# Kernel tuning notes

Measured on AMD Instinct MI355X. Metric: run time of the kernel, lower is better.

Reference implementation:

```python
import jax, jax.numpy as jnp
import numpy as np

NUM_HEADS = 8
LN_EPS = 1e-5


def layer_norm(x, g, b):
    mu = jnp.mean(x, axis=-1, keepdims=True)
    var = jnp.var(x, axis=-1, keepdims=True)
    return (x - mu) * jax.lax.rsqrt(var + LN_EPS) * g + b


def mha(q, k, v, in_w, in_b, out_w, out_b):
    # torch nn.MultiheadAttention (batch_first): packed in_proj (3D,D), out_proj (D,D)
    B, Lq, D = q.shape
    Lk = k.shape[1]
    H = NUM_HEADS
    dh = D // H
    wq, wk, wv = in_w[:D], in_w[D:2 * D], in_w[2 * D:]
    bq, bk, bv = in_b[:D], in_b[D:2 * D], in_b[2 * D:]
    qp = (q @ wq.T + bq).reshape(B, Lq, H, dh).transpose(0, 2, 1, 3)
    kp = (k @ wk.T + bk).reshape(B, Lk, H, dh).transpose(0, 2, 1, 3)
    vp = (v @ wv.T + bv).reshape(B, Lk, H, dh).transpose(0, 2, 1, 3)
    scores = jnp.einsum('bhqd,bhkd->bhqk', qp, kp) / jnp.sqrt(jnp.asarray(dh, q.dtype))
    attn = jax.nn.softmax(scores, axis=-1)  # (B,H,Lq,Lk)
    out = jnp.einsum('bhqk,bhkd->bhqd', attn, vp)
    out = out.transpose(0, 2, 1, 3).reshape(B, Lq, D)
    return out @ out_w.T + out_b, attn


def setup_inputs() -> dict:
    key = jax.random.key(0)
    ks = jax.random.split(key, 8)
    B, P, Q, D = 32, 576, 256, 768
    s = 0.02
    return {
        'image_tokens': jax.random.normal(ks[0], (B, 1 + P, D), jnp.float32),
        'tactile_tokens': jax.random.normal(ks[1], (B, Q, D), jnp.float32),
        't2i_in_w': jax.random.normal(ks[2], (3 * D, D), jnp.float32) * s,
        't2i_in_b': jnp.zeros((3 * D,), jnp.float32),
        't2i_out_w': jax.random.normal(ks[3], (D, D), jnp.float32) * s,
        't2i_out_b': jnp.zeros((D,), jnp.float32),
        'i2t_in_w': jax.random.normal(ks[4], (3 * D, D), jnp.float32) * s,
        'i2t_in_b': jnp.zeros((3 * D,), jnp.float32),
        'i2t_out_w': jax.random.normal(ks[5], (D, D), jnp.float32) * s,
        'i2t_out_b': jnp.zeros((D,), jnp.float32),
        'ln_tact_g': jnp.ones((D,), jnp.float32),
        'ln_tact_b': jnp.zeros((D,), jnp.float32),
        'ln_img_g': jnp.ones((D,), jnp.float32),
        'ln_img_b': jnp.zeros((D,), jnp.float32),
    }


def reference(image_tokens, tactile_tokens, t2i_in_w, t2i_in_b, t2i_out_w, t2i_out_b,
              i2t_in_w, i2t_in_b, i2t_out_w, i2t_out_b,
              ln_tact_g, ln_tact_b, ln_img_g, ln_img_b):
    # attention_type == 'all_patch'
    cls_tok = image_tokens[:, :1, :]
    patch_tok = image_tokens[:, 1:, :]
    tact_out, attn_weights = mha(tactile_tokens, patch_tok, patch_tok,
                                 t2i_in_w, t2i_in_b, t2i_out_w, t2i_out_b)
    tactile_tokens = layer_norm(tactile_tokens + tact_out, ln_tact_g, ln_tact_b)
    patch_out, _ = mha(patch_tok, tactile_tokens, tactile_tokens,
                       i2t_in_w, i2t_in_b, i2t_out_w, i2t_out_b)
    patch_tok = layer_norm(patch_tok + patch_out, ln_img_g, ln_img_b)
    image_tokens = jnp.concatenate([cls_tok, patch_tok], axis=1)
    return image_tokens, tactile_tokens, attn_weights
```

## Files before the change

### kernel.cpp

```cpp
#include <hip/hip_runtime.h>
#include <stdint.h>
#include <math.h>

typedef unsigned short u16;
typedef __attribute__((ext_vector_type(8))) short bf16x8;
typedef __attribute__((ext_vector_type(4))) float f32x4;

__device__ __forceinline__ u16 f2b(float f) {
    unsigned u = __float_as_uint(f);
    u = (u + 0x7FFFu + ((u >> 16) & 1u)) >> 16;
    return (u16)u;
}

__device__ __forceinline__ void gload16(const void* g, void* lds) {
    __builtin_amdgcn_global_load_lds(
        (const __attribute__((address_space(1))) unsigned int*)(uintptr_t)g,
        (__attribute__((address_space(3))) unsigned int*)(unsigned int)(uintptr_t)lds,
        16, 0, 0);
}

#define BM 128
#define BN 128
#define BK 32

struct GemmGrp {
    const u16* A; const u16* B; const float* bias; const float* resid;
    float* Cf; u16* Cb;
    int M, N, lda, ldb, ldc;
    float scale;
    int rgrp; long long rgA, rgoff; int ldr;
};
struct G3 { GemmGrp g[3]; int start[4]; int K; };

__global__ __launch_bounds__(256) void gemm_grp(G3 P)
{
    __shared__ __align__(16) u16 lA[2][BM * BK];
    __shared__ __align__(16) u16 lB[2][BN * BK];

    const int tid = threadIdx.x;
    const int wave = tid >> 6;
    const int lane = tid & 63;

    const int ntot = P.start[3];
    int L = blockIdx.x;
    if ((ntot & 7) == 0) L = (L & 7) * (ntot >> 3) + (L >> 3);

    const int gi = (L >= P.start[1]) + (L >= P.start[2]);
    GemmGrp g;
    if (gi == 0) g = P.g[0]; else if (gi == 1) g = P.g[1]; else g = P.g[2];
    const int t = L - P.start[gi];

    const int tilesN = g.N / BN;
    const int tm = t / tilesN;
    const int tn = t % tilesN;
    const int row0 = tm * BM;
    const int col0 = tn * BN;

    const int f0 = tid * 8;
    const int f1 = (256 + tid) * 8;
    const int sr0 = f0 >> 5, sc0 = f0 & 31;
    const int sr1 = f1 >> 5, sc1 = f1 & 31;

    const u16* pa0 = g.A + (long long)(row0 + sr0) * g.lda + sc0;
    const u16* pa1 = g.A + (long long)(row0 + sr1) * g.lda + sc1;
    const u16* pb0 = g.B + (long long)(col0 + sr0) * g.ldb + sc0;
    const u16* pb1 = g.B + (long long)(col0 + sr1) * g.ldb + sc1;

    const int wr = wave >> 1, wc = wave & 1;
    const int fr = lane & 15;
    const int kk = (lane >> 4) * 8;

    f32x4 acc[4][4];
    #pragma unroll
    for (int m = 0; m < 4; ++m)
        #pragma unroll
        for (int n = 0; n < 4; ++n) {
            f32x4 z = {0.f, 0.f, 0.f, 0.f};
            acc[m][n] = z;
        }

    #define STAGE(buf, k0) do { \
        gload16(pa0 + (k0), &lA[buf][(wave * 64) * 8]); \
        gload16(pa1 + (k0), &lA[buf][2048 + (wave * 64) * 8]); \
        gload16(pb0 + (k0), &lB[buf][(wave * 64) * 8]); \
        gload16(pb1 + (k0), &lB[buf][2048 + (wave * 64) * 8]); \
    } while (0)

    STAGE(0, 0);
    __syncthreads();
    int cur = 0;
    for (int k0 = 0; k0 < P.K; k0 += BK) {
        if (k0 + BK < P.K) STAGE(cur ^ 1, k0 + BK);
        bf16x8 af[4], bfv[4];
        #pragma unroll
        for (int m = 0; m < 4; ++m)
            af[m] = *(const bf16x8*)&lA[cur][(wr * 64 + m * 16 + fr) * BK + kk];
        #pragma unroll
        for (int n = 0; n < 4; ++n)
            bfv[n] = *(const bf16x8*)&lB[cur][(wc * 64 + n * 16 + fr) * BK + kk];
        #pragma unroll
        for (int m = 0; m < 4; ++m)
            #pragma unroll
            for (int n = 0; n < 4; ++n)
                acc[m][n] = __builtin_amdgcn_mfma_f32_16x16x32_bf16(af[m], bfv[n], acc[m][n], 0, 0, 0);
        __syncthreads();
        cur ^= 1;
    }
    #undef STAGE

    const int orow = row0 + wr * 64;
    const int ocol = col0 + wc * 64;
    const int g4 = (lane >> 4) * 4;
    float bcol[4];
    #pragma unroll
    for (int n = 0; n < 4; ++n)
        bcol[n] = g.bias ? g.bias[ocol + n * 16 + fr] : 0.f;

    #pragma unroll
    for (int m = 0; m < 4; ++m) {
        #pragma unroll
        for (int j = 0; j < 4; ++j) {
            const int r = orow + m * 16 + g4 + j;
            long long ro = 0;
            if (g.resid) {
                unsigned q = (unsigned)r / (unsigned)g.rgrp;
                unsigned rem = (unsigned)r - q * (unsigned)g.rgrp;
                ro = (long long)q * g.rgA + (long long)rem * g.ldr + g.rgoff;
            }
            const long long crow = (long long)r * g.ldc;
            #pragma unroll
            for (int n = 0; n < 4; ++n) {
                const int c = ocol + n * 16 + fr;
                float v = acc[m][n][j] * g.scale + bcol[n];
                if (g.resid) v += g.resid[ro + c];
                if (g.Cb) g.Cb[crow + c] = f2b(v);
                else      g.Cf[crow + c] = v;
            }
        }
    }
}

template <bool WATTN>
__global__ __launch_bounds__(256, 2) void fused_attn(
    const u16* __restrict__ Q, const u16* __restrict__ K, const u16* __restrict__ Vt,
    float* __restrict__ attn, u16* __restrict__ O,
    int Lq, int Lk, int ldq, int ldk, int ldo)
{
    __shared__ __align__(16) u16 lQP[128 * 96];
    __shared__ __align__(16) u16 lKt[2][64 * 96];
    __shared__ __align__(16) u16 lVt[2][96 * 64];
    __shared__ float lM2[2][128], lL2[2][128];

    const int tid = threadIdx.x, wave = tid >> 6, lane = tid & 63;
    const int fr = lane & 15, g = lane >> 4;
    const int wr = wave >> 1, wc = wave & 1;
    const int z = blockIdx.y, b = z >> 3, h = z & 7;
    const int q0 = blockIdx.x * 128;
    const int nt = Lk >> 6;

    const u16* Qz = Q + (long long)b * Lq * ldq + h * 96;
    const u16* Kz = K + (long long)b * Lk * ldk + h * 96;
    const u16* Vz = Vt + (long long)z * 96 * Lk;
    u16* Oz = O + (long long)b * Lq * ldo + h * 96;
    float* Az = attn + (long long)z * Lq * Lk;

    const u16* qsrc[6];
    #pragma unroll
    for (int t = 0; t < 6; ++t) {
        int u = t * 256 + tid;
        int r = u / 12, cu = u % 12;
        int qr = q0 + r; if (qr > Lq - 1) qr = Lq - 1;
        qsrc[t] = Qz + (long long)qr * ldq + cu * 8;
    }
    const u16* ksrc[3];
    #pragma unroll
    for (int t = 0; t < 3; ++t) {
        int u = t * 256 + tid;
        int r = u / 12, cu = u % 12;
        ksrc[t] = Kz + (long long)r * ldk + cu * 8;
    }
    const u16* vsrc[3];
    #pragma unroll
    for (int t = 0; t < 3; ++t) {
        int u = t * 256 + tid;
        int d = u >> 3, uu = u & 7;
        vsrc[t] = Vz + (long long)d * Lk + ((uu ^ (d & 7)) * 8);
    }
    const long long kstep = 64LL * ldk;

    #define DQ(t)    ((char*)lQP + ((t) * 256 + wave * 64) * 16)
    #define DK(bf,t) ((char*)lKt[bf] + ((t) * 256 + wave * 64) * 16)
    #define DV(bf,t) ((char*)lVt[bf] + ((t) * 256 + wave * 64) * 16)

    #pragma unroll
    for (int t = 0; t < 6; ++t) gload16(qsrc[t], DQ(t));
    #pragma unroll
    for (int t = 0; t < 3; ++t) gload16(ksrc[t], DK(0, t));
    __syncthreads();

    bf16x8 qf[4][3];
    #pragma unroll
    for (int m = 0; m < 4; ++m)
        #pragma unroll
        for (int ks = 0; ks < 3; ++ks)
            qf[m][ks] = *(const bf16x8*)((const char*)lQP + (wr * 64 + m * 16 + fr) * 192 + ks * 64 + g * 16);

    float m_run[4], l_run[4];
    #pragma unroll
    for (int i = 0; i < 4; ++i) { m_run[i] = -1e30f; l_run[i] = 0.f; }

    int buf = 0;
    for (int i = 0; i < nt; ++i) {
        if (i + 1 < nt) {
            #pragma unroll
            for (int t = 0; t < 3; ++t) { ksrc[t] += kstep; gload16(ksrc[t], DK(buf ^ 1, t)); }
        }
        bf16x8 kf[2][3];
        #pragma unroll
        for (int mk = 0; mk < 2; ++mk)
            #pragma unroll
            for (int ks = 0; ks < 3; ++ks)
                kf[mk][ks] = *(const bf16x8*)((const char*)lKt[buf] + (wc * 32 + mk * 16 + fr) * 192 + ks * 64 + g * 16);
        f32x4 sa[2][4];
        #pragma unroll
        for (int mk = 0; mk < 2; ++mk)
            #pragma unroll
            for (int nq = 0; nq < 4; ++nq) {
                f32x4 zz = {0.f, 0.f, 0.f, 0.f};
                sa[mk][nq] = zz;
            }
        __builtin_amdgcn_s_setprio(1);
        #pragma unroll
        for (int ks = 0; ks < 3; ++ks)
            #pragma unroll
            for (int mk = 0; mk < 2; ++mk)
                #pragma unroll
                for (int nq = 0; nq < 4; ++nq)
                    sa[mk][nq] = __builtin_amdgcn_mfma_f32_16x16x32_bf16(kf[mk][ks], qf[nq][ks], sa[mk][nq], 0, 0, 0);
        __builtin_amdgcn_s_setprio(0);
        #pragma unroll
        for (int nq = 0; nq < 4; ++nq) {
            float tmx = -1e30f;
            #pragma unroll
            for (int mk = 0; mk < 2; ++mk)
                #pragma unroll
                for (int j = 0; j < 4; ++j)
                    tmx = fmaxf(tmx, sa[mk][nq][j]);
            tmx = fmaxf(tmx, __shfl_xor(tmx, 16));
            tmx = fmaxf(tmx, __shfl_xor(tmx, 32));
            const float mnew = fmaxf(m_run[nq], tmx);
            float ts = 0.f;
            #pragma unroll
            for (int mk = 0; mk < 2; ++mk)
                #pragma unroll
                for (int j = 0; j < 4; ++j)
                    ts += __expf(sa[mk][nq][j] - mnew);
            ts += __shfl_xor(ts, 16);
            ts += __shfl_xor(ts, 32);
            l_run[nq] = l_run[nq] * __expf(m_run[nq] - mnew) + ts;
            m_run[nq] = mnew;
        }
        __syncthreads();
        buf ^= 1;
    }

    if (g == 0) {
        #pragma unroll
        for (int nq = 0; nq < 4; ++nq) {
            lM2[wc][wr * 64 + nq * 16 + fr] = m_run[nq];
            lL2[wc][wr * 64 + nq * 16 + fr] = l_run[nq];
        }
    }
    #pragma unroll
    for (int t = 0; t < 3; ++t) ksrc[t] -= (long long)(nt - 1) * kstep;
    #pragma unroll
    for (int t = 0; t < 3; ++t) gload16(ksrc[t], DK(0, t));
    #pragma unroll
    for (int t = 0; t < 3; ++t) gload16(vsrc[t], DV(0, t));
    __syncthreads();

    float mrow[16], linv[16];
    #pragma unroll
    for (int m = 0; m < 4; ++m)
        #pragma unroll
        for (int j = 0; j < 4; ++j) {
            const int q = wr * 64 + m * 16 + g * 4 + j;
            const float ma = lM2[0][q], mb = lM2[1][q];
            const float mm = fmaxf(ma, mb);
            const float ll = lL2[0][q] * __expf(ma - mm) + lL2[1][q] * __expf(mb - mm);
            mrow[m * 4 + j] = mm;
            linv[m * 4 + j] = 1.f / ll;
        }

    f32x4 oacc[4][3];
    #pragma unroll
    for (int m = 0; m < 4; ++m)
        #pragma unroll
        for (int nd = 0; nd < 3; ++nd) {
            f32x4 zz = {0.f, 0.f, 0.f, 0.f};
            oacc[m][nd] = zz;
        }

    buf = 0;
    for (int i = 0; i < nt; ++i) {
        const int k0 = i * 64;
        if (i + 1 < nt) {
            #pragma unroll
            for (int t = 0; t < 3; ++t) { ksrc[t] += kstep; gload16(ksrc[t], DK(buf ^ 1, t)); }
            #pragma unroll
            for (int t = 0; t < 3; ++t) { vsrc[t] += 64;    gload16(vsrc[t], DV(buf ^ 1, t)); }
        }
        bf16x8 kf[2][3];
        #pragma unroll
        for (int n = 0; n < 2; ++n)
            #pragma unroll
            for (int ks = 0; ks < 3; ++ks)
                kf[n][ks] = *(const bf16x8*)((const char*)lKt[buf] + (wc * 32 + n * 16 + fr) * 192 + ks * 64 + g * 16);
        f32x4 ss[4][2];
        #pragma unroll
        for (int m = 0; m < 4; ++m)
            #pragma unroll
            for (int n = 0; n < 2; ++n) {
                f32x4 zz = {0.f, 0.f, 0.f, 0.f};
                ss[m][n] = zz;
            }
        __builtin_amdgcn_s_setprio(1);
        #pragma unroll
        for (int ks = 0; ks < 3; ++ks)
            #pragma unroll
            for (int m = 0; m < 4; ++m)
                #pragma unroll
                for (int n = 0; n < 2; ++n)
                    ss[m][n] = __builtin_amdgcn_mfma_f32_16x16x32_bf16(qf[m][ks], kf[n][ks], ss[m][n], 0, 0, 0);
        __builtin_amdgcn_s_setprio(0);
        #pragma unroll
        for (int m = 0; m < 4; ++m)
            #pragma unroll
            for (int n = 0; n < 2; ++n)
                #pragma unroll
                for (int j = 0; j < 4; ++j) {
                    const float p = __expf(ss[m][n][j] - mrow[m * 4 + j]) * linv[m * 4 + j];
                    const int q = wr * 64 + m * 16 + g * 4 + j;
                    const int k = wc * 32 + n * 16 + fr;
                    if (WATTN) Az[(long long)(q0 + q) * Lk + k0 + k] = p;
                    *(u16*)((char*)lQP + q * 144 + k * 2) = f2b(p);
                }
        __syncthreads();
        __builtin_amdgcn_s_setprio(1);
        #pragma unroll
        for (int ks = 0; ks < 2; ++ks) {
            bf16x8 vf[3], pf[4];
            #pragma unroll
            for (int nd = 0; nd < 3; ++nd) {
                const int row = wc * 48 + nd * 16 + fr;
                vf[nd] = *(const bf16x8*)((const char*)lVt[buf] + row * 128 + (((ks * 4 + g) ^ (row & 7)) * 16));
            }
            #pragma unroll
            for (int m = 0; m < 4; ++m)
                pf[m] = *(const bf16x8*)((const char*)lQP + (wr * 64 + m * 16 + fr) * 144 + ks * 64 + g * 16);
            #pragma unroll
            for (int m = 0; m < 4; ++m)
                #pragma unroll
                for (int nd = 0; nd < 3; ++nd)
                    oacc[m][nd] = __builtin_amdgcn_mfma_f32_16x16x32_bf16(pf[m], vf[nd], oacc[m][nd], 0, 0, 0);
        }
        __builtin_amdgcn_s_setprio(0);
        __syncthreads();
        buf ^= 1;
    }

    #pragma unroll
    for (int m = 0; m < 4; ++m)
        #pragma unroll
        for (int j = 0; j < 4; ++j) {
            const int q = q0 + wr * 64 + m * 16 + g * 4 + j;
            if (q < Lq) {
                #pragma unroll
                for (int nd = 0; nd < 3; ++nd) {
                    const int c = wc * 48 + nd * 16 + fr;
                    Oz[(long long)q * ldo + c] = f2b(oacc[m][nd][j]);
                }
            }
        }
    #undef DQ
    #undef DK
    #undef DV
}

__global__ __launch_bounds__(256) void transpose_v(
    const u16* __restrict__ V, u16* __restrict__ Vt, int L, int ldv)
{
    __shared__ unsigned int t[64 * 97];
    const int z = blockIdx.y;
    const int b = z >> 3, h = z & 7;
    const int l0 = blockIdx.x * 64;
    const int tid = threadIdx.x;
    for (int i = 0; i < 24; ++i) {
        const int idx = tid + i * 256;
        const int l = idx / 96, d = idx % 96;
        t[l * 97 + d] = V[((long long)(b * L + l0 + l)) * ldv + h * 96 + d];
    }
    __syncthreads();
    for (int i = 0; i < 24; ++i) {
        const int idx = tid + i * 256;
        const int d = idx / 64, l = idx % 64;
        Vt[((long long)z * 96 + d) * L + l0 + l] = (u16)t[l * 97 + d];
    }
}

__global__ __launch_bounds__(256) void ln_k(
    const float* __restrict__ X, const float* __restrict__ g, const float* __restrict__ b,
    float* __restrict__ outF, u16* __restrict__ outB,
    int rows, int grp, long long gA, long long goff, int ldo)
{
    const int wave = threadIdx.x >> 6, lane = threadIdx.x & 63;
    const int row = blockIdx.x * 4 + wave;
    if (row >= rows) return;
    const float* x = X + (long long)row * 768;
    float v[12], s = 0.f, sq = 0.f;
    #pragma unroll
    for (int i = 0; i < 12; ++i) { v[i] = x[lane + 64 * i]; s += v[i]; sq += v[i] * v[i]; }
    #pragma unroll
    for (int o = 32; o; o >>= 1) { s += __shfl_xor(s, o); sq += __shfl_xor(sq, o); }
    const float mu = s * (1.f / 768.f);
    const float var = sq * (1.f / 768.f) - mu * mu;
    const float inv = rsqrtf(var + 1e-5f);
    const long long ob = (long long)(row / grp) * gA + (long long)(row % grp) * ldo + goff;
    #pragma unroll
    for (int i = 0; i < 12; ++i) {
        const int c = lane + 64 * i;
        const float y = (v[i] - mu) * inv * g[c] + b[c];
        outF[ob + c] = y;
        if (outB) outB[(long long)row * 768 + c] = f2b(y);
    }
}

__global__ __launch_bounds__(256) void conv_f2b(
    const float4* __restrict__ in, u16* __restrict__ out, long long n4)
{
    long long i = (long long)blockIdx.x * 256 + threadIdx.x;
    const long long stride = (long long)gridDim.x * 256;
    for (; i < n4; i += stride) {
        const float4 f = in[i];
        ushort4 u;
        u.x = f2b(f.x); u.y = f2b(f.y); u.z = f2b(f.z); u.w = f2b(f.w);
        ((ushort4*)out)[i] = u;
    }
}

__global__ __launch_bounds__(256) void conv_w4(
    const float4* __restrict__ a, const float4* __restrict__ b,
    const float4* __restrict__ c, const float4* __restrict__ d,
    u16* __restrict__ oa, u16* __restrict__ ob,
    u16* __restrict__ oc, u16* __restrict__ od)
{
    const long long n1 = 442368, n2 = 589824, n3 = 1032192, n4 = 1179648;
    long long i = (long long)blockIdx.x * 256 + threadIdx.x;
    const long long stride = (long long)gridDim.x * 256;
    for (; i < n4; i += stride) {
        const float4* src; u16* dst; long long k;
        if (i < n1)      { src = a; dst = oa; k = i; }
        else if (i < n2) { src = b; dst = ob; k = i - n1; }
        else if (i < n3) { src = c; dst = oc; k = i - n2; }
        else             { src = d; dst = od; k = i - n3; }
        const float4 f = src[k];
        ushort4 u;
        u.x = f2b(f.x); u.y = f2b(f.y); u.z = f2b(f.z); u.w = f2b(f.w);
        ((ushort4*)dst)[k] = u;
    }
}

__global__ __launch_bounds__(256) void conv_patch(
    const float* __restrict__ img, u16* __restrict__ out)
{
    long long i = (long long)blockIdx.x * 256 + threadIdx.x;
    const long long n4 = 18432LL * 192;
    const long long stride = (long long)gridDim.x * 256;
    for (; i < n4; i += stride) {
        const long long r = i / 192; const int c4 = (int)(i % 192);
        const long long sr = (r / 576) * 577 + 1 + (r % 576);
        const float4 f = ((const float4*)img)[sr * 192 + c4];
        ushort4 u;
        u.x = f2b(f.x); u.y = f2b(f.y); u.z = f2b(f.z); u.w = f2b(f.w);
        ((ushort4*)out)[i] = u;
    }
}

__global__ __launch_bounds__(256) void cls_copy(
    const float* __restrict__ img, float* __restrict__ out)
{
    const int i = blockIdx.x * 256 + threadIdx.x;
    if (i < 32 * 768) {
        const int b = i / 768, c = i % 768;
        out[(long long)b * 577 * 768 + c] = img[(long long)b * 577 * 768 + c];
    }
}

static inline GemmGrp mkgrp(const u16* A, const u16* B, const float* bias,
    const float* resid, float* Cf, u16* Cb, int M, int N, int lda, int ldb,
    int ldc, float scale, int rgrp, long long rgA, long long rgoff, int ldr)
{
    GemmGrp g;
    g.A = A; g.B = B; g.bias = bias; g.resid = resid; g.Cf = Cf; g.Cb = Cb;
    g.M = M; g.N = N; g.lda = lda; g.ldb = ldb; g.ldc = ldc;
    g.scale = scale; g.rgrp = rgrp; g.rgA = rgA; g.rgoff = rgoff; g.ldr = ldr;
    return g;
}

static inline void launch_grp(hipStream_t s, const GemmGrp* gs, int ng, int K)
{
    G3 P;
    P.start[0] = 0;
    for (int i = 0; i < 3; ++i) {
        const GemmGrp& src = gs[i < ng ? i : ng - 1];
        P.g[i] = src;
        const int nb = (i < ng) ? (src.M / BM) * (src.N / BN) : 0;
        P.start[i + 1] = P.start[i] + nb;
    }
    P.K = K;
    gemm_grp<<<dim3((unsigned)P.start[3]), dim3(256), 0, s>>>(P);
}

extern "C" void kernel_launch(void* const* d_in, const int* in_sizes, int n_in,
                              void* d_out, int out_size, void* d_ws, size_t ws_size,
                              hipStream_t stream)
{
    (void)in_sizes; (void)n_in; (void)out_size; (void)ws_size;
    const float* img   = (const float*)d_in[0];
    const float* tac   = (const float*)d_in[1];
    const float* w1in  = (const float*)d_in[2];
    const float* b1in  = (const float*)d_in[3];
    const float* w1out = (const float*)d_in[4];
    const float* b1out = (const float*)d_in[5];
    const float* w2in  = (const float*)d_in[6];
    const float* b2in  = (const float*)d_in[7];
    const float* w2out = (const float*)d_in[8];
    const float* b2out = (const float*)d_in[9];
    const float* lng1  = (const float*)d_in[10];
    const float* lnb1  = (const float*)d_in[11];
    const float* lng2  = (const float*)d_in[12];
    const float* lnb2  = (const float*)d_in[13];
    float* out = (float*)d_out;

    const long long o_tac  = 32LL * 577 * 768;
    const long long o_attn = o_tac + 32LL * 256 * 768;
    const float qscale = 1.0f / sqrtf(96.0f);

    u16* p = (u16*)d_ws;
    u16* tact_bf    = p; p += 8192LL * 768;
    u16* patch_bf   = p; p += 18432LL * 768;
    u16* w1in_bf    = p; p += 2304LL * 768;
    u16* w1out_bf   = p; p += 768LL * 768;
    u16* w2in_bf    = p; p += 2304LL * 768;
    u16* w2out_bf   = p; p += 768LL * 768;
    u16* tactnew_bf = p; p += 8192LL * 768;
    u16* Q1  = p; p += 8192LL * 768;
    u16* KV1 = p; p += 18432LL * 1536;
    u16* Vt1 = p; p += 256LL * 96 * 576;
    u16* AO1 = p; p += 8192LL * 768;
    u16* Q2  = p; p += 18432LL * 768;
    u16* KV2 = p; p += 8192LL * 1536;
    u16* Vt2 = p; p += 256LL * 96 * 256;
    u16* AO2 = p; p += 18432LL * 768;
    float* O1s = (float*)p; p += 2LL * 8192 * 768;
    float* O2s = (float*)p; p += 2LL * 18432 * 768;

    conv_f2b<<<1024, 256, 0, stream>>>((const float4*)tac, tact_bf, 8192LL * 192);
    conv_patch<<<1024, 256, 0, stream>>>(img, patch_bf);
    conv_w4<<<1024, 256, 0, stream>>>(
        (const float4*)w1in, (const float4*)w1out, (const float4*)w2in, (const float4*)w2out,
        w1in_bf, w1out_bf, w2in_bf, w2out_bf);
    cls_copy<<<96, 256, 0, stream>>>(img, out);

    {
        GemmGrp gs[3] = {
            mkgrp(tact_bf,  w1in_bf,              b1in,       nullptr, nullptr, Q1,
                  8192, 768, 768, 768, 768, qscale, 1, 0, 0, 0),
            mkgrp(patch_bf, w1in_bf + 768LL*768,  b1in + 768, nullptr, nullptr, KV1,
                  18432, 1536, 768, 768, 1536, 1.0f, 1, 0, 0, 0),
            mkgrp(patch_bf, w2in_bf,              b2in,       nullptr, nullptr, Q2,
                  18432, 768, 768, 768, 768, qscale, 1, 0, 0, 0)
        };
        launch_grp(stream, gs, 3, 768);
    }

    transpose_v<<<dim3(9, 256), 256, 0, stream>>>(KV1 + 768, Vt1, 576, 1536);
    fused_attn<true><<<dim3(2, 256), 256, 0, stream>>>(
        Q1, KV1, Vt1, out + o_attn, AO1, 256, 576, 768, 1536, 768);
    {
        GemmGrp g = mkgrp(AO1, w1out_bf, b1out, tac, O1s, nullptr,
                          8192, 768, 768, 768, 768, 1.0f, 1, 768, 0, 0);
        launch_grp(stream, &g, 1, 768);
    }
    ln_k<<<8192 / 4, 256, 0, stream>>>(O1s, lng1, lnb1, out + o_tac, tactnew_bf,
        8192, 8192, 0, 0, 768);

    {
        GemmGrp g = mkgrp(tactnew_bf, w2in_bf + 768LL*768, b2in + 768, nullptr,
                          nullptr, KV2, 8192, 1536, 768, 768, 1536, 1.0f, 1, 0, 0, 0);
        launch_grp(stream, &g, 1, 768);
    }
    transpose_v<<<dim3(4, 256), 256, 0, stream>>>(KV2 + 768, Vt2, 256, 1536);
    fused_attn<false><<<dim3(5, 256), 256, 0, stream>>>(
        Q2, KV2, Vt2, nullptr, AO2, 576, 256, 768, 1536, 768);
    {
        GemmGrp g = mkgrp(AO2, w2out_bf, b2out, img, O2s, nullptr,
                          18432, 768, 768, 768, 768, 1.0f, 576, 577LL * 768, 768, 768);
        launch_grp(stream, &g, 1, 768);
    }
    ln_k<<<18432 / 4, 256, 0, stream>>>(O2s, lng2, lnb2, out, nullptr,
        18432, 576, 577LL * 768, 768, 768);
}
```

Before: 763.8 us.

## Add single-pass online-softmax flash attention for second cross-attention

Adds a single-pass flash_attn kernel for the image-to-tactile attention, where attention weights are not needed. It uses an online softmax with a lazy rescale threshold in place of the two-pass fused kernel, which reads K twice. Each wave now owns 32 query rows and the full 96-wide head dimension. The prefetch of the next K/V tile (and the GEMM stage load) is also moved after the current tile's LDS fragment reads. The first attention stays on fused_attn with its template parameter removed.

```diff
diff --git a/kernel.cpp b/kernel.cpp
--- a/kernel.cpp
+++ b/kernel.cpp
@@ -90,7 +90,6 @@
     __syncthreads();
     int cur = 0;
     for (int k0 = 0; k0 < P.K; k0 += BK) {
-        if (k0 + BK < P.K) STAGE(cur ^ 1, k0 + BK);
         bf16x8 af[4], bfv[4];
         #pragma unroll
         for (int m = 0; m < 4; ++m)
@@ -98,6 +97,7 @@
         #pragma unroll
         for (int n = 0; n < 4; ++n)
             bfv[n] = *(const bf16x8*)&lB[cur][(wc * 64 + n * 16 + fr) * BK + kk];
+        if (k0 + BK < P.K) STAGE(cur ^ 1, k0 + BK);
         #pragma unroll
         for (int m = 0; m < 4; ++m)
             #pragma unroll
@@ -140,7 +140,6 @@
     }
 }
 
-template <bool WATTN>
 __global__ __launch_bounds__(256, 2) void fused_attn(
     const u16* __restrict__ Q, const u16* __restrict__ K, const u16* __restrict__ Vt,
     float* __restrict__ attn, u16* __restrict__ O,
@@ -211,16 +210,16 @@
 
     int buf = 0;
     for (int i = 0; i < nt; ++i) {
-        if (i + 1 < nt) {
-            #pragma unroll
-            for (int t = 0; t < 3; ++t) { ksrc[t] += kstep; gload16(ksrc[t], DK(buf ^ 1, t)); }
-        }
         bf16x8 kf[2][3];
         #pragma unroll
         for (int mk = 0; mk < 2; ++mk)
             #pragma unroll
             for (int ks = 0; ks < 3; ++ks)
                 kf[mk][ks] = *(const bf16x8*)((const char*)lKt[buf] + (wc * 32 + mk * 16 + fr) * 192 + ks * 64 + g * 16);
+        if (i + 1 < nt) {
+            #pragma unroll
+            for (int t = 0; t < 3; ++t) { ksrc[t] += kstep; gload16(ksrc[t], DK(buf ^ 1, t)); }
+        }
         f32x4 sa[2][4];
         #pragma unroll
         for (int mk = 0; mk < 2; ++mk)
@@ -304,18 +303,18 @@
     buf = 0;
     for (int i = 0; i < nt; ++i) {
         const int k0 = i * 64;
-        if (i + 1 < nt) {
-            #pragma unroll
-            for (int t = 0; t < 3; ++t) { ksrc[t] += kstep; gload16(ksrc[t], DK(buf ^ 1, t)); }
-            #pragma unroll
-            for (int t = 0; t < 3; ++t) { vsrc[t] += 64;    gload16(vsrc[t], DV(buf ^ 1, t)); }
-        }
         bf16x8 kf[2][3];
         #pragma unroll
         for (int n = 0; n < 2; ++n)
             #pragma unroll
             for (int ks = 0; ks < 3; ++ks)
                 kf[n][ks] = *(const bf16x8*)((const char*)lKt[buf] + (wc * 32 + n * 16 + fr) * 192 + ks * 64 + g * 16);
+        if (i + 1 < nt) {
+            #pragma unroll
+            for (int t = 0; t < 3; ++t) { ksrc[t] += kstep; gload16(ksrc[t], DK(buf ^ 1, t)); }
+            #pragma unroll
+            for (int t = 0; t < 3; ++t) { vsrc[t] += 64;    gload16(vsrc[t], DV(buf ^ 1, t)); }
+        }
         f32x4 ss[4][2];
         #pragma unroll
         for (int m = 0; m < 4; ++m)
@@ -342,7 +341,7 @@
                     const float p = __expf(ss[m][n][j] - mrow[m * 4 + j]) * linv[m * 4 + j];
                     const int q = wr * 64 + m * 16 + g * 4 + j;
                     const int k = wc * 32 + n * 16 + fr;
-                    if (WATTN) Az[(long long)(q0 + q) * Lk + k0 + k] = p;
+                    Az[(long long)(q0 + q) * Lk + k0 + k] = p;
                     *(u16*)((char*)lQP + q * 144 + k * 2) = f2b(p);
                 }
         __syncthreads();
@@ -380,6 +379,188 @@
                     const int c = wc * 48 + nd * 16 + fr;
                     Oz[(long long)q * ldo + c] = f2b(oacc[m][nd][j]);
                 }
+            }
+        }
+    #undef DQ
+    #undef DK
+    #undef DV
+}
+
+__global__ __launch_bounds__(256, 2) void flash_attn(
+    const u16* __restrict__ Q, const u16* __restrict__ K, const u16* __restrict__ Vt,
+    u16* __restrict__ O, int Lq, int Lk, int ldq, int ldk, int ldo)
+{
+    __shared__ __align__(16) u16 lQP[128 * 96];
+    __shared__ __align__(16) u16 lKt[2][64 * 96];
+    __shared__ __align__(16) u16 lVt[2][96 * 64];
+
+    const int tid = threadIdx.x, wave = tid >> 6, lane = tid & 63;
+    const int fr = lane & 15, g = lane >> 4;
+    const int z = blockIdx.y, b = z >> 3, h = z & 7;
+    const int q0 = blockIdx.x * 128;
+    const int nt = Lk >> 6;
+
+    const u16* Qz = Q + (long long)b * Lq * ldq + h * 96;
+    const u16* Kz = K + (long long)b * Lk * ldk + h * 96;
+    const u16* Vz = Vt + (long long)z * 96 * Lk;
+    u16* Oz = O + (long long)b * Lq * ldo + h * 96;
+
+    const u16* qsrc[6];
+    #pragma unroll
+    for (int t = 0; t < 6; ++t) {
+        int u = t * 256 + tid;
+        int r = u / 12, cu = u % 12;
+        int qr = q0 + r; if (qr > Lq - 1) qr = Lq - 1;
+        qsrc[t] = Qz + (long long)qr * ldq + cu * 8;
+    }
+    const u16* ksrc[3];
+    #pragma unroll
+    for (int t = 0; t < 3; ++t) {
+        int u = t * 256 + tid;
+        int r = u / 12, cu = u % 12;
+        ksrc[t] = Kz + (long long)r * ldk + cu * 8;
+    }
+    const u16* vsrc[3];
+    #pragma unroll
+    for (int t = 0; t < 3; ++t) {
+        int u = t * 256 + tid;
+        int d = u >> 3, uu = u & 7;
+        vsrc[t] = Vz + (long long)d * Lk + ((uu ^ (d & 7)) * 8);
+    }
+    const long long kstep = 64LL * ldk;
+
+    #define DQ(t)    ((char*)lQP + ((t) * 256 + wave * 64) * 16)
+    #define DK(bf,t) ((char*)lKt[bf] + ((t) * 256 + wave * 64) * 16)
+    #define DV(bf,t) ((char*)lVt[bf] + ((t) * 256 + wave * 64) * 16)
+
+    #pragma unroll
+    for (int t = 0; t < 6; ++t) gload16(qsrc[t], DQ(t));
+    #pragma unroll
+    for (int t = 0; t < 3; ++t) gload16(ksrc[t], DK(0, t));
+    #pragma unroll
+    for (int t = 0; t < 3; ++t) gload16(vsrc[t], DV(0, t));
+    __syncthreads();
+
+    bf16x8 qf[2][3];
+    #pragma unroll
+    for (int m = 0; m < 2; ++m)
+        #pragma unroll
+        for (int ks = 0; ks < 3; ++ks)
+            qf[m][ks] = *(const bf16x8*)((const char*)lQP + (wave * 32 + m * 16 + fr) * 192 + ks * 64 + g * 16);
+
+    float m_run[2][4], l_run[2][4];
+    #pragma unroll
+    for (int m = 0; m < 2; ++m)
+        #pragma unroll
+        for (int j = 0; j < 4; ++j) { m_run[m][j] = -1e30f; l_run[m][j] = 0.f; }
+
+    f32x4 oacc[2][6];
+    #pragma unroll
+    for (int m = 0; m < 2; ++m)
+        #pragma unroll
+        for (int nd = 0; nd < 6; ++nd) {
+            f32x4 zz = {0.f, 0.f, 0.f, 0.f};
+            oacc[m][nd] = zz;
+        }
+
+    int buf = 0;
+    for (int i = 0; i < nt; ++i) {
+        bf16x8 kf[4][3];
+        #pragma unroll
+        for (int n = 0; n < 4; ++n)
+            #pragma unroll
+            for (int ks = 0; ks < 3; ++ks)
+                kf[n][ks] = *(const bf16x8*)((const char*)lKt[buf] + (n * 16 + fr) * 192 + ks * 64 + g * 16);
+        if (i + 1 < nt) {
+            #pragma unroll
+            for (int t = 0; t < 3; ++t) { ksrc[t] += kstep; gload16(ksrc[t], DK(buf ^ 1, t)); }
+            #pragma unroll
+            for (int t = 0; t < 3; ++t) { vsrc[t] += 64;    gload16(vsrc[t], DV(buf ^ 1, t)); }
+        }
+        f32x4 ss[2][4];
+        #pragma unroll
+        for (int m = 0; m < 2; ++m)
+            #pragma unroll
+            for (int n = 0; n < 4; ++n) {
+                f32x4 zz = {0.f, 0.f, 0.f, 0.f};
+                ss[m][n] = zz;
+            }
+        __builtin_amdgcn_s_setprio(1);
+        #pragma unroll
+        for (int ks = 0; ks < 3; ++ks)
+            #pragma unroll
+            for (int m = 0; m < 2; ++m)
+                #pragma unroll
+                for (int n = 0; n < 4; ++n)
+                    ss[m][n] = __builtin_amdgcn_mfma_f32_16x16x32_bf16(qf[m][ks], kf[n][ks], ss[m][n], 0, 0, 0);
+        __builtin_amdgcn_s_setprio(0);
+
+        #pragma unroll
+        for (int m = 0; m < 2; ++m)
+            #pragma unroll
+            for (int j = 0; j < 4; ++j) {
+                float pm = fmaxf(fmaxf(ss[m][0][j], ss[m][1][j]), fmaxf(ss[m][2][j], ss[m][3][j]));
+                pm = fmaxf(pm, __shfl_xor(pm, 1));
+                pm = fmaxf(pm, __shfl_xor(pm, 2));
+                pm = fmaxf(pm, __shfl_xor(pm, 4));
+                pm = fmaxf(pm, __shfl_xor(pm, 8));
+                const float mo = m_run[m][j];
+                const bool up = pm > mo + 8.0f;
+                const float mnew = up ? pm : mo;
+                const float sc = up ? __expf(mo - mnew) : 1.0f;
+                m_run[m][j] = mnew;
+                l_run[m][j] *= sc;
+                #pragma unroll
+                for (int nd = 0; nd < 6; ++nd) oacc[m][nd][j] *= sc;
+                const int row = wave * 32 + m * 16 + g * 4 + j;
+                float ls = 0.f;
+                #pragma unroll
+                for (int n = 0; n < 4; ++n) {
+                    const float p = __expf(ss[m][n][j] - mnew);
+                    ls += p;
+                    *(u16*)((char*)lQP + row * 144 + (n * 16 + fr) * 2) = f2b(p);
+                }
+                l_run[m][j] += ls;
+            }
+
+        __builtin_amdgcn_s_setprio(1);
+        #pragma unroll
+        for (int ks = 0; ks < 2; ++ks) {
+            bf16x8 pf[2], vf[6];
+            #pragma unroll
+            for (int m = 0; m < 2; ++m)
+                pf[m] = *(const bf16x8*)((const char*)lQP + (wave * 32 + m * 16 + fr) * 144 + ks * 64 + g * 16);
+            #pragma unroll
+            for (int nd = 0; nd < 6; ++nd) {
+                const int row = nd * 16 + fr;
+                vf[nd] = *(const bf16x8*)((const char*)lVt[buf] + row * 128 + (((ks * 4 + g) ^ (row & 7)) * 16));
+            }
+            #pragma unroll
+            for (int m = 0; m < 2; ++m)
+                #pragma unroll
+                for (int nd = 0; nd < 6; ++nd)
+                    oacc[m][nd] = __builtin_amdgcn_mfma_f32_16x16x32_bf16(pf[m], vf[nd], oacc[m][nd], 0, 0, 0);
+        }
+        __builtin_amdgcn_s_setprio(0);
+        __syncthreads();
+        buf ^= 1;
+    }
+
+    #pragma unroll
+    for (int m = 0; m < 2; ++m)
+        #pragma unroll
+        for (int j = 0; j < 4; ++j) {
+            float l = l_run[m][j];
+            l += __shfl_xor(l, 1);
+            l += __shfl_xor(l, 2);
+            l += __shfl_xor(l, 4);
+            l += __shfl_xor(l, 8);
+            const float inv = 1.f / l;
+            const int q = q0 + wave * 32 + m * 16 + g * 4 + j;
+            if (q < Lq) {
+                #pragma unroll
+                for (int nd = 0; nd < 6; ++nd)
+                    Oz[(long long)q * ldo + nd * 16 + fr] = f2b(oacc[m][nd][j] * inv);
             }
         }
     #undef DQ
@@ -585,7 +766,7 @@
     }
 
     transpose_v<<<dim3(9, 256), 256, 0, stream>>>(KV1 + 768, Vt1, 576, 1536);
-    fused_attn<true><<<dim3(2, 256), 256, 0, stream>>>(
+    fused_attn<<<dim3(2, 256), 256, 0, stream>>>(
         Q1, KV1, Vt1, out + o_attn, AO1, 256, 576, 768, 1536, 768);
     {
         GemmGrp g = mkgrp(AO1, w1out_bf, b1out, tac, O1s, nullptr,
@@ -601,8 +782,8 @@
         launch_grp(stream, &g, 1, 768);
     }
     transpose_v<<<dim3(4, 256), 256, 0, stream>>>(KV2 + 768, Vt2, 256, 1536);
-    fused_attn<false><<<dim3(5, 256), 256, 0, stream>>>(
-        Q2, KV2, Vt2, nullptr, AO2, 576, 256, 768, 1536, 768);
+    flash_attn<<<dim3(5, 256), 256, 0, stream>>>(
+        Q2, KV2, Vt2, AO2, 576, 256, 768, 1536, 768);
     {
         GemmGrp g = mkgrp(AO2, w2out_bf, b2out, img, O2s, nullptr,
                           18432, 768, 768, 768, 768, 1.0f, 576, 577LL * 768, 768, 768);
```

Result: no change. 764.0 us (+0.0%).
